# Kernel optimization log

Hardware: AMD Instinct MI355X
Metric: run time of the kernel (lower is better)

## Reference

```python
import jax, jax.numpy as jnp
import numpy as np

D_MODEL = 512
N_PAIRS = D_MODEL // 2
B, T = 8, 4096


def setup_inputs() -> dict:
    key = jax.random.key(0)
    ks = jax.random.split(key, 7)
    scale = 1.0 / np.sqrt(D_MODEL)
    return {
        "x_seq": jax.random.normal(ks[0], (B, T, D_MODEL), dtype=jnp.float32),
        "W_angle": jax.random.uniform(ks[1], (D_MODEL, N_PAIRS), jnp.float32, -scale, scale),
        "b_angle": jnp.zeros((N_PAIRS,), jnp.float32),
        "W_decay": jax.random.uniform(ks[2], (D_MODEL, 1), jnp.float32, -scale, scale),
        "b_decay": jnp.full((1,), 1.4, jnp.float32),
        "W_input": jax.random.uniform(ks[3], (D_MODEL, D_MODEL), jnp.float32, -scale, scale),
        "b_input": jax.random.uniform(ks[4], (D_MODEL,), jnp.float32, -scale, scale),
    }


def _givens_ssm(x_seq, W_angle, b_angle, W_decay, b_decay, W_input, b_input):
    Bb, Tt, D = x_seq.shape
    P = D // 2
    angles = jnp.einsum("btd,dp->btp", x_seq, W_angle) + b_angle          # [B,T,P]
    decays = jax.nn.sigmoid(jnp.einsum("btd,dk->btk", x_seq, W_decay) + b_decay)[..., 0]  # [B,T]
    inj = jnp.einsum("btd,de->bte", x_seq, W_input) + b_input              # [B,T,D]
    inj = inj.reshape(Bb, Tt, P, 2)

    # scan over time: h_t = decay_t * Rot(angles_t) h_{t-1} + inj_t, pairwise 2x2 rotations
    def step(h, inp):
        a, d, u = inp  # a:[B,P], d:[B], u:[B,P,2]
        c, s = jnp.cos(a), jnp.sin(a)
        he = c * h[..., 0] - s * h[..., 1]
        ho = s * h[..., 0] + c * h[..., 1]
        h_new = d[:, None, None] * jnp.stack([he, ho], axis=-1) + u
        return h_new, h_new

    h0 = jnp.zeros((Bb, P, 2), x_seq.dtype)
    xs = (jnp.swapaxes(angles, 0, 1), jnp.swapaxes(decays, 0, 1), jnp.swapaxes(inj, 0, 1))
    _, states = jax.lax.scan(step, h0, xs)  # [T,B,P,2]
    return jnp.swapaxes(states, 0, 1).reshape(Bb, Tt, D)


def reference(x_seq, W_angle, b_angle, W_decay, b_decay, W_input, b_input):
    return _givens_ssm(x_seq, W_angle, b_angle, W_decay, b_decay, W_input, b_input)
```

## Files before the change

### kernel.cpp

```cpp
#include <hip/hip_runtime.h>
#include <math.h>

typedef _Float16 half_t;
typedef __attribute__((ext_vector_type(8))) _Float16 half8;
typedef __attribute__((ext_vector_type(2))) _Float16 half2v;
typedef __attribute__((ext_vector_type(4))) float floatx4;

#define BATCH   8
#define SEQ     4096
#define DM      512
#define NP      256
#define M_TOT   32768
#define NTOT    768
#define CHUNKS  256
#define CHUNK_LEN 16

__device__ __forceinline__ void async_load16(const void* g, void* l) {
    __builtin_amdgcn_global_load_lds((const __attribute__((address_space(1))) void*)g,
                                     (__attribute__((address_space(3))) void*)l,
                                     16, 0, 0);
}

__global__ __launch_bounds__(256) void decay_convert(const float* __restrict__ X,
                                                     const float* __restrict__ Wd,
                                                     const float* __restrict__ bd,
                                                     float* __restrict__ dec,
                                                     half_t* __restrict__ Xh) {
    const int wave = threadIdx.x >> 6;
    const int lane = threadIdx.x & 63;
    const int row0 = blockIdx.x * 8 + wave * 2;
    const float4* x0 = (const float4*)(X + (size_t)row0 * DM);
    const float4* x1 = x0 + 128;
    const float4* wd = (const float4*)Wd;
    float4 a0 = x0[2 * lane], a1 = x0[2 * lane + 1];
    float4 b0 = x1[2 * lane], b1 = x1[2 * lane + 1];
    float4 w0 = wd[2 * lane], w1 = wd[2 * lane + 1];
    float s0 = a0.x * w0.x + a0.y * w0.y + a0.z * w0.z + a0.w * w0.w
             + a1.x * w1.x + a1.y * w1.y + a1.z * w1.z + a1.w * w1.w;
    float s1 = b0.x * w0.x + b0.y * w0.y + b0.z * w0.z + b0.w * w0.w
             + b1.x * w1.x + b1.y * w1.y + b1.z * w1.z + b1.w * w1.w;
    half8 h0 = {(half_t)a0.x, (half_t)a0.y, (half_t)a0.z, (half_t)a0.w,
                (half_t)a1.x, (half_t)a1.y, (half_t)a1.z, (half_t)a1.w};
    half8 h1 = {(half_t)b0.x, (half_t)b0.y, (half_t)b0.z, (half_t)b0.w,
                (half_t)b1.x, (half_t)b1.y, (half_t)b1.z, (half_t)b1.w};
    *(half8*)(Xh + (size_t)row0 * DM + lane * 8) = h0;
    *(half8*)(Xh + (size_t)(row0 + 1) * DM + lane * 8) = h1;
#pragma unroll
    for (int off = 32; off > 0; off >>= 1) {
        s0 += __shfl_down(s0, off, 64);
        s1 += __shfl_down(s1, off, 64);
    }
    if (lane == 0) {
        dec[row0]     = 1.0f / (1.0f + __expf(-(s0 + bd[0])));
        dec[row0 + 1] = 1.0f / (1.0f + __expf(-(s1 + bd[0])));
    }
}

__global__ __launch_bounds__(256) void wcat_transpose(const float* __restrict__ Wi,
                                                      const float* __restrict__ Wa,
                                                      half_t* __restrict__ Wt) {
    const int idx = blockIdx.x * 256 + threadIdx.x;
    const int n = idx >> 9;
    const int k = idx & 511;
    float v = (n < DM) ? Wi[(size_t)k * DM + n] : Wa[(size_t)k * NP + (n - DM)];
    Wt[idx] = (half_t)v;
}

__global__ __launch_bounds__(256) void gemm_fused(const half_t* __restrict__ Xh,
                                                  const half_t* __restrict__ Wt,
                                                  const float* __restrict__ bi,
                                                  const float* __restrict__ ba,
                                                  float* __restrict__ out,
                                                  half_t* __restrict__ angles) {
    __shared__ __align__(16) char As[8192];
    __shared__ __align__(16) char Bs[8192];

    const int bm   = blockIdx.x;
    const int bn   = blockIdx.y;
    const int tid  = threadIdx.x;
    const int wave = tid >> 6;
    const int lane = tid & 63;
    const int quad = lane >> 4;
    const int l16  = lane & 15;
    const int wrow = wave >> 1;
    const int wcol = wave & 1;

    floatx4 acc[4][4];
#pragma unroll
    for (int i = 0; i < 4; ++i)
#pragma unroll
        for (int j = 0; j < 4; ++j) acc[i][j] = (floatx4){0.f, 0.f, 0.f, 0.f};

    const int s0 = wave * 128 + lane;
    const int s1 = s0 + 64;
    const int r0 = s0 >> 2, kql0 = (s0 & 3) ^ ((r0 >> 1) & 3);
    const int r1 = s1 >> 2, kql1 = (s1 & 3) ^ ((r1 >> 1) & 3);
    const half_t* gA0 = Xh + (size_t)(bm * 128 + r0) * DM + kql0 * 8;
    const half_t* gA1 = Xh + (size_t)(bm * 128 + r1) * DM + kql1 * 8;
    const half_t* gB0 = Wt + (size_t)(bn * 128 + r0) * DM + kql0 * 8;
    const half_t* gB1 = Wt + (size_t)(bn * 128 + r1) * DM + kql1 * 8;
    char* lA0 = As + wave * 2048;
    char* lA1 = As + wave * 2048 + 1024;
    char* lB0 = Bs + wave * 2048;
    char* lB1 = Bs + wave * 2048 + 1024;

    for (int k0 = 0; k0 < DM; k0 += 32) {
        async_load16(gA0 + k0, lA0);
        async_load16(gA1 + k0, lA1);
        async_load16(gB0 + k0, lB0);
        async_load16(gB1 + k0, lB1);
        __syncthreads();

        half8 af[4], bf[4];
#pragma unroll
        for (int mt = 0; mt < 4; ++mt) {
            const int r = wrow * 64 + mt * 16 + l16;
            af[mt] = *(const half8*)(As + r * 64 + ((quad ^ ((r >> 1) & 3)) << 4));
        }
#pragma unroll
        for (int nt = 0; nt < 4; ++nt) {
            const int r = wcol * 64 + nt * 16 + l16;
            bf[nt] = *(const half8*)(Bs + r * 64 + ((quad ^ ((r >> 1) & 3)) << 4));
        }
#pragma unroll
        for (int mt = 0; mt < 4; ++mt)
#pragma unroll
            for (int nt = 0; nt < 4; ++nt)
                acc[mt][nt] = __builtin_amdgcn_mfma_f32_16x16x32_f16(af[mt], bf[nt],
                                                                     acc[mt][nt], 0, 0, 0);
        __syncthreads();
    }

    const int colbase = bn * 128 + wcol * 64;
#pragma unroll
    for (int nt = 0; nt < 4; ++nt) {
        const int col = colbase + nt * 16 + l16;
        const bool is_inj = col < DM;
        const float bias = is_inj ? bi[col] : ba[col - DM];
#pragma unroll
        for (int mt = 0; mt < 4; ++mt) {
            const int rowb = bm * 128 + wrow * 64 + mt * 16 + quad * 4;
#pragma unroll
            for (int r = 0; r < 4; ++r) {
                const float v = acc[mt][nt][r] + bias;
                const int row = rowb + r;
                if (is_inj) out[(size_t)row * DM + col] = v;
                else        angles[(size_t)row * NP + (col - DM)] = (half_t)v;
            }
        }
    }
}

__global__ __launch_bounds__(256) void scan_sum1(const half_t* __restrict__ angles,
                                                 const float* __restrict__ decays,
                                                 const float* __restrict__ inj,
                                                 float* __restrict__ thetaC,
                                                 float4* __restrict__ hend,
                                                 float* __restrict__ Dprod) {
    const int b   = blockIdx.x >> 7;
    const int sub = threadIdx.x >> 7;
    const int th  = threadIdx.x & 127;
    const int c   = (blockIdx.x & 127) * 2 + sub;
    const int p0  = th * 2;
    const int t0  = c * CHUNK_LEN;

    const half_t* ap = angles + (size_t)(b * SEQ + t0) * NP + p0;
    const float4* up = (const float4*)inj + (size_t)(b * SEQ + t0) * 128 + (p0 >> 1);
    const float*  dp = decays + b * SEQ + t0;

    half2v ab[2][8]; float4 ub[2][8]; float db[2][8];
#pragma unroll
    for (int j = 0; j < 8; ++j) {
        ab[0][j] = *(const half2v*)(ap + (size_t)j * NP);
        ub[0][j] = up[(size_t)j * 128];
        db[0][j] = dp[j];
    }

    float h0a = 0, h1a = 0, h0b = 0, h1b = 0, tha = 0, thb = 0, dc = 1.0f;
#pragma unroll
    for (int g = 0; g < 2; ++g) {
        const int cur = g & 1, nxt = cur ^ 1;
        if (g < 1) {
#pragma unroll
            for (int j = 0; j < 8; ++j) {
                const int t = (g + 1) * 8 + j;
                ab[nxt][j] = *(const half2v*)(ap + (size_t)t * NP);
                ub[nxt][j] = up[(size_t)t * 128];
                db[nxt][j] = dp[t];
            }
        }
#pragma unroll
        for (int j = 0; j < 8; ++j) {
            float a0 = (float)ab[cur][j][0], a1 = (float)ab[cur][j][1];
            float4 u = ub[cur][j];
            float d  = db[cur][j];
            float s0, c0, s1, c1;
            __sincosf(a0, &s0, &c0);
            __sincosf(a1, &s1, &c1);
            float n0a = fmaf(d, c0 * h0a - s0 * h1a, u.x);
            float n1a = fmaf(d, s0 * h0a + c0 * h1a, u.y);
            float n0b = fmaf(d, c1 * h0b - s1 * h1b, u.z);
            float n1b = fmaf(d, s1 * h0b + c1 * h1b, u.w);
            h0a = n0a; h1a = n1a; h0b = n0b; h1b = n1b;
            tha += a0; thb += a1; dc *= d;
        }
    }
    const size_t cbase = (size_t)(b * CHUNKS + c) * NP + p0;
    *(float2*)(thetaC + cbase) = make_float2(tha, thb);
    hend[cbase >> 1] = make_float4(h0a, h1a, h0b, h1b);
    if (th == 0) Dprod[b * CHUNKS + c] = dc;
}

__global__ __launch_bounds__(256) void scan_chunks(const float* __restrict__ thetaC,
                                                   const float4* __restrict__ hend,
                                                   const float* __restrict__ Dprod,
                                                   float4* __restrict__ hentry) {
    const int b  = blockIdx.x >> 7;
    const int pp = blockIdx.x & 127;
    const int c  = threadIdx.x;

    __shared__ float  sTa[256], sTb[256], sD[256];
    __shared__ float4 sV[256];

    const size_t idx = (size_t)(b * CHUNKS + c);
    const float2 th2 = *(const float2*)(thetaC + idx * NP + pp * 2);
    float4 v = hend[idx * 128 + pp];
    float  D = Dprod[idx];
    float tha = th2.x, thb = th2.y;

    sTa[c] = tha; sTb[c] = thb; sD[c] = D; sV[c] = v;

#pragma unroll
    for (int o = 1; o < 256; o <<= 1) {
        __syncthreads();
        float lta = 0.f, ltb = 0.f, lD = 0.f;
        float4 lv = make_float4(0.f, 0.f, 0.f, 0.f);
        const bool has = (c >= o);
        if (has) { lta = sTa[c - o]; ltb = sTb[c - o]; lD = sD[c - o]; lv = sV[c - o]; }
        __syncthreads();
        if (has) {
            float s0, c0, s1, c1;
            __sincosf(tha, &s0, &c0);
            __sincosf(thb, &s1, &c1);
            v.x = fmaf(D, c0 * lv.x - s0 * lv.y, v.x);
            v.y = fmaf(D, s0 * lv.x + c0 * lv.y, v.y);
            v.z = fmaf(D, c1 * lv.z - s1 * lv.w, v.z);
            v.w = fmaf(D, s1 * lv.z + c1 * lv.w, v.w);
            tha += lta; thb += ltb; D *= lD;
            sTa[c] = tha; sTb[c] = thb; sD[c] = D; sV[c] = v;
        }
    }
    __syncthreads();
    const float4 e = (c == 0) ? make_float4(0.f, 0.f, 0.f, 0.f) : sV[c - 1];
    hentry[idx * 128 + pp] = e;
}

__global__ __launch_bounds__(256) void scan_final(const half_t* __restrict__ angles,
                                                  const float* __restrict__ decays,
                                                  const float4* __restrict__ hentry,
                                                  float* __restrict__ out) {
    const int b   = blockIdx.x >> 7;
    const int sub = threadIdx.x >> 7;
    const int th  = threadIdx.x & 127;
    const int c   = (blockIdx.x & 127) * 2 + sub;
    const int p0  = th * 2;
    const int t0  = c * CHUNK_LEN;

    const half_t* ap = angles + (size_t)(b * SEQ + t0) * NP + p0;
    float4*       op = (float4*)out + (size_t)(b * SEQ + t0) * 128 + (p0 >> 1);
    const float*  dp = decays + b * SEQ + t0;

    float4 v = hentry[(size_t)(b * CHUNKS + c) * 128 + (p0 >> 1)];
    float h0a = v.x, h1a = v.y, h0b = v.z, h1b = v.w;

    half2v ab[2][8]; float4 ub[2][8]; float db[2][8];
#pragma unroll
    for (int j = 0; j < 8; ++j) {
        ab[0][j] = *(const half2v*)(ap + (size_t)j * NP);
        ub[0][j] = op[(size_t)j * 128];
        db[0][j] = dp[j];
    }

#pragma unroll
    for (int g = 0; g < 2; ++g) {
        const int cur = g & 1, nxt = cur ^ 1;
        if (g < 1) {
#pragma unroll
            for (int j = 0; j < 8; ++j) {
                const int t = (g + 1) * 8 + j;
                ab[nxt][j] = *(const half2v*)(ap + (size_t)t * NP);
                ub[nxt][j] = op[(size_t)t * 128];
                db[nxt][j] = dp[t];
            }
        }
#pragma unroll
        for (int j = 0; j < 8; ++j) {
            const int t = g * 8 + j;
            float a0 = (float)ab[cur][j][0], a1 = (float)ab[cur][j][1];
            float4 u = ub[cur][j];
            float d  = db[cur][j];
            float s0, c0, s1, c1;
            __sincosf(a0, &s0, &c0);
            __sincosf(a1, &s1, &c1);
            float n0a = fmaf(d, c0 * h0a - s0 * h1a, u.x);
            float n1a = fmaf(d, s0 * h0a + c0 * h1a, u.y);
            float n0b = fmaf(d, c1 * h0b - s1 * h1b, u.z);
            float n1b = fmaf(d, s1 * h0b + c1 * h1b, u.w);
            h0a = n0a; h1a = n1a; h0b = n0b; h1b = n1b;
            op[(size_t)t * 128] = make_float4(h0a, h1a, h0b, h1b);
        }
    }
}

extern "C" void kernel_launch(void* const* d_in, const int* in_sizes, int n_in,
                              void* d_out, int out_size, void* d_ws, size_t ws_size,
                              hipStream_t stream) {
    const float* x  = (const float*)d_in[0];
    const float* Wa = (const float*)d_in[1];
    const float* ba = (const float*)d_in[2];
    const float* Wd = (const float*)d_in[3];
    const float* bd = (const float*)d_in[4];
    const float* Wi = (const float*)d_in[5];
    const float* bi = (const float*)d_in[6];
    float* out = (float*)d_out;

    char* ws = (char*)d_ws;
    half_t* x_h     = (half_t*)(ws);
    float*  thetaC  = (float*)(ws);
    float4* hend    = (float4*)(ws + 2097152);
    float*  Dprod   = (float*)(ws + 6291456);
    float4* hentry  = (float4*)(ws + 6299648);
    half_t* angles  = (half_t*)(ws + 33554432);
    float*  decays  = (float*)(ws + 50331648);
    half_t* Wcat_t  = (half_t*)(ws + 50462720);

    decay_convert<<<M_TOT / 8, 256, 0, stream>>>(x, Wd, bd, decays, x_h);
    wcat_transpose<<<(NTOT * DM) / 256, 256, 0, stream>>>(Wi, Wa, Wcat_t);
    gemm_fused<<<dim3(M_TOT / 128, NTOT / 128), 256, 0, stream>>>(x_h, Wcat_t, bi, ba, out, angles);

    scan_sum1<<<BATCH * CHUNKS / 2, 256, 0, stream>>>(angles, decays, out, thetaC, hend, Dprod);
    scan_chunks<<<BATCH * 128, 256, 0, stream>>>(thetaC, hend, Dprod, hentry);
    scan_final<<<BATCH * CHUNKS / 2, 256, 0, stream>>>(angles, decays, hentry, out);
}
```

Measured before the change: 220.5 us.

## Double-buffer LDS tiles in fused GEMM with async prefetch of next K slice

The fused projection GEMM now uses two LDS buffers per operand. It issues the global-to-LDS loads for the next K step before waiting on the current one, using explicit vmcnt waits and raw barriers in place of __syncthreads. The goal is to overlap global memory latency with MFMA work. In exchange LDS use doubles to 32KB per block, which may reduce occupancy. Correctness also depends on the manual waitcnt accounting and on LDS reads completing before the trailing barrier.

```diff
diff --git a/kernel.cpp b/kernel.cpp
--- a/kernel.cpp
+++ b/kernel.cpp
@@ -72,8 +72,8 @@
                                                   const float* __restrict__ ba,
                                                   float* __restrict__ out,
                                                   half_t* __restrict__ angles) {
-    __shared__ __align__(16) char As[8192];
-    __shared__ __align__(16) char Bs[8192];
+    __shared__ __align__(16) char As[2][8192];
+    __shared__ __align__(16) char Bs[2][8192];
 
     const int bm   = blockIdx.x;
     const int bn   = blockIdx.y;
@@ -99,28 +99,42 @@
     const half_t* gA1 = Xh + (size_t)(bm * 128 + r1) * DM + kql1 * 8;
     const half_t* gB0 = Wt + (size_t)(bn * 128 + r0) * DM + kql0 * 8;
     const half_t* gB1 = Wt + (size_t)(bn * 128 + r1) * DM + kql1 * 8;
-    char* lA0 = As + wave * 2048;
-    char* lA1 = As + wave * 2048 + 1024;
-    char* lB0 = Bs + wave * 2048;
-    char* lB1 = Bs + wave * 2048 + 1024;
-
-    for (int k0 = 0; k0 < DM; k0 += 32) {
-        async_load16(gA0 + k0, lA0);
-        async_load16(gA1 + k0, lA1);
-        async_load16(gB0 + k0, lB0);
-        async_load16(gB1 + k0, lB1);
-        __syncthreads();
-
+    const int woff = wave * 2048;
+
+    async_load16(gA0, As[0] + woff);
+    async_load16(gA1, As[0] + woff + 1024);
+    async_load16(gB0, Bs[0] + woff);
+    async_load16(gB1, Bs[0] + woff + 1024);
+
+#pragma unroll
+    for (int step = 0; step < 16; ++step) {
+        const int cur = step & 1;
+        const int nxt = cur ^ 1;
+        if (step < 15) {
+            const int kn = (step + 1) * 32;
+            async_load16(gA0 + kn, As[nxt] + woff);
+            async_load16(gA1 + kn, As[nxt] + woff + 1024);
+            async_load16(gB0 + kn, Bs[nxt] + woff);
+            async_load16(gB1 + kn, Bs[nxt] + woff + 1024);
+            asm volatile("s_waitcnt vmcnt(4)" ::: "memory");
+        } else {
+            asm volatile("s_waitcnt vmcnt(0)" ::: "memory");
+        }
+        __builtin_amdgcn_s_barrier();
+        __builtin_amdgcn_sched_barrier(0);
+
+        const char* Ab = As[cur];
+        const char* Bb = Bs[cur];
         half8 af[4], bf[4];
 #pragma unroll
         for (int mt = 0; mt < 4; ++mt) {
             const int r = wrow * 64 + mt * 16 + l16;
-            af[mt] = *(const half8*)(As + r * 64 + ((quad ^ ((r >> 1) & 3)) << 4));
+            af[mt] = *(const half8*)(Ab + r * 64 + ((quad ^ ((r >> 1) & 3)) << 4));
         }
 #pragma unroll
         for (int nt = 0; nt < 4; ++nt) {
             const int r = wcol * 64 + nt * 16 + l16;
-            bf[nt] = *(const half8*)(Bs + r * 64 + ((quad ^ ((r >> 1) & 3)) << 4));
+            bf[nt] = *(const half8*)(Bb + r * 64 + ((quad ^ ((r >> 1) & 3)) << 4));
         }
 #pragma unroll
         for (int mt = 0; mt < 4; ++mt)
@@ -128,7 +142,7 @@
             for (int nt = 0; nt < 4; ++nt)
                 acc[mt][nt] = __builtin_amdgcn_mfma_f32_16x16x32_f16(af[mt], bf[nt],
                                                                      acc[mt][nt], 0, 0, 0);
-        __syncthreads();
+        __builtin_amdgcn_s_barrier();
     }
 
     const int colbase = bn * 128 + wcol * 64;
```

Result: no change. 220.4 us (-0.0%).
